# Kernel tuning notes

Measured on AMD Instinct MI355X. Metric: run time of the kernel, lower is better.

Reference implementation:

```python
import jax, jax.numpy as jnp
import numpy as np

B, S, D, H = 2, 2048, 1024, 16
HD = D // H  # head_dim = 64


def setup_inputs() -> dict:
    key = jax.random.key(0)
    ks = jax.random.split(key, 12)
    xav = (2.0 / (D + D)) ** 0.5  # xavier_normal std for square Linear
    q = jax.random.normal(ks[0], (B, S, D), jnp.float32)
    k = jax.random.normal(ks[1], (B, S, D), jnp.float32)
    v = jax.random.normal(ks[2], (B, S, D), jnp.float32)
    Wq = jax.random.normal(ks[3], (D, D), jnp.float32) * xav
    Wk = jax.random.normal(ks[4], (D, D), jnp.float32) * xav
    Wv = jax.random.normal(ks[5], (D, D), jnp.float32) * xav
    bq = jnp.zeros((D,), jnp.float32)
    bk = jnp.zeros((D,), jnp.float32)
    bv = jnp.zeros((D,), jnp.float32)
    # valid-prefix padding masks (True = valid token); key 0 always valid so
    # no causal softmax row is fully masked (avoids NaN, matches real usage).
    klen = jax.random.randint(ks[6], (B,), S // 2, S + 1)
    qlen = jax.random.randint(ks[7], (B,), S // 2, S + 1)
    pos = jnp.arange(S)
    key_padding_mask = pos[None, :] < klen[:, None]
    query_padding_mask = pos[None, :] < qlen[:, None]
    return {
        "q": q, "k": k, "v": v,
        "Wq": Wq, "bq": bq, "Wk": Wk, "bk": bk, "Wv": Wv, "bv": bv,
        "key_padding_mask": key_padding_mask,
        "query_padding_mask": query_padding_mask,
    }


def _proj_split(x, W, b, n_heads):
    # Linear (y = x W^T + b) then split heads: [B,S,D] -> [B,H,S,hd]
    bsz, sq, dm = x.shape
    hd = dm // n_heads
    y = x @ W.T + b
    return y.reshape(bsz, sq, n_heads, hd).transpose(0, 2, 1, 3)


def reference(q, k, v, Wq, bq, Wk, bk, Wv, bv, key_padding_mask, query_padding_mask):
    bsz, sq, dm = q.shape
    sk = k.shape[1]
    Q = _proj_split(q, Wq, bq, H)  # [B,H,Sq,hd]
    K = _proj_split(k, Wk, bk, H)  # [B,H,Sk,hd]
    V = _proj_split(v, Wv, bv, H)  # [B,H,Sk,hd]
    scale = 1.0 / jnp.sqrt(jnp.asarray(Q.shape[-1], Q.dtype))
    scores = jnp.einsum('bhqd,bhkd->bhqk', Q, K) * scale  # [B,H,Sq,Sk]
    # key padding: -inf where key invalid
    scores = jnp.where(key_padding_mask[:, None, None, :], scores, -jnp.inf)
    # causal: -inf strictly above the diagonal
    causal_ok = jnp.tril(jnp.ones((sq, sk), bool))
    scores = jnp.where(causal_ok[None, None, :, :], scores, -jnp.inf)
    attn = jax.nn.softmax(scores, axis=-1)
    # q_mask: zero out rows for padded queries (post-softmax, as in source)
    attn = jnp.where(query_padding_mask[:, None, :, None], attn, 0.0)
    # dropout p=0.0 -> identity
    out = jnp.einsum('bhqk,bhkd->bhqd', attn, V)
    out = out.transpose(0, 2, 1, 3).reshape(bsz, sq, dm)
    return out + q
```

## Files before the change

kernel.cpp:

```cpp
#include <hip/hip_runtime.h>
#include <stdint.h>

#define BATCH 2
#define SEQ 2048
#define DMODEL 1024
#define NHEAD 16
#define HDIM 64
#define CVT_BLOCKS 15360

typedef __attribute__((ext_vector_type(8))) short bf16x8;
typedef __attribute__((ext_vector_type(4))) float f32x4;

__device__ __forceinline__ unsigned short f2bf(float f) {
  unsigned int u = __float_as_uint(f);
  u += 0x7fffu + ((u >> 16) & 1u);
  return (unsigned short)(u >> 16);
}
__device__ __forceinline__ unsigned int pk2bf(float a, float b) {
  return __builtin_amdgcn_perm(__float_as_uint(b) + 0x8000u,
                               __float_as_uint(a) + 0x8000u, 0x07060302u);
}
__device__ __forceinline__ void async_copy16(const void* g, void* l) {
  __builtin_amdgcn_global_load_lds(
      (const __attribute__((address_space(1))) void*)g,
      (__attribute__((address_space(3))) void*)l, 16, 0, 0);
}

__global__ __launch_bounds__(256) void cvt_all(
    const float* __restrict__ q, const float* __restrict__ k,
    const float* __restrict__ v, const float* __restrict__ Wq,
    const float* __restrict__ Wk, const float* __restrict__ Wv,
    unsigned short* __restrict__ dst,
    const unsigned char* __restrict__ kp, const unsigned char* __restrict__ qp,
    int* __restrict__ lens) {
  if (blockIdx.x == CVT_BLOCKS) {
    const int t = threadIdx.x, wave = t >> 6, lane = t & 63;
    const unsigned char* base = (wave < 2) ? kp : qp;
    const int b = wave & 1;
    const bool bytefmt = (base[1] != 0);
    int cnt = 0;
    if (bytefmt) {
      const uint4* p = (const uint4*)(base + (size_t)b * SEQ);
#pragma unroll
      for (int g = 0; g < 2; g++) {
        const uint4 x = p[g * 64 + lane];
        const unsigned int w[4] = {x.x, x.y, x.z, x.w};
#pragma unroll
        for (int i = 0; i < 4; i++) {
          const unsigned int ww = w[i];
          cnt += ((ww & 0xffu) != 0) + ((ww & 0xff00u) != 0) +
                 ((ww & 0xff0000u) != 0) + ((ww & 0xff000000u) != 0);
        }
      }
    } else {
      const uint4* p = (const uint4*)(base + (size_t)b * SEQ * 4);
#pragma unroll
      for (int g = 0; g < 8; g++) {
        const uint4 x = p[g * 64 + lane];
        cnt += (x.x != 0) + (x.y != 0) + (x.z != 0) + (x.w != 0);
      }
    }
#pragma unroll
    for (int off = 32; off >= 1; off >>= 1) cnt += __shfl_xor(cnt, off, 64);
    if (lane == 0) lens[wave] = cnt;
    return;
  }
  const int g = blockIdx.x * 256 + threadIdx.x;
  const float* src;
  size_t off, dbase;
  if (g < 3 * (1 << 20)) {
    const int ti = g >> 20;
    src = (ti == 0) ? q : (ti == 1) ? k : v;
    off = (size_t)(g & ((1 << 20) - 1));
    dbase = (size_t)ti << 22;
  } else {
    const int gw = g - 3 * (1 << 20);
    const int ti = gw >> 18;
    src = (ti == 0) ? Wq : (ti == 1) ? Wk : Wv;
    off = (size_t)(gw & ((1 << 18) - 1));
    dbase = (3ull << 22) + ((size_t)ti << 20);
  }
  const float4 x = ((const float4*)src)[off];
  ushort4 o;
  o.x = f2bf(x.x); o.y = f2bf(x.y); o.z = f2bf(x.z); o.w = f2bf(x.w);
  *(ushort4*)(dst + dbase + off * 4) = o;
}

__global__ __launch_bounds__(256) void qkv_proj(
    const unsigned short* __restrict__ xq, const unsigned short* __restrict__ xk,
    const unsigned short* __restrict__ xv,
    const unsigned short* __restrict__ Wq, const float* __restrict__ bq,
    const unsigned short* __restrict__ Wk, const float* __restrict__ bk,
    const unsigned short* __restrict__ Wv, const float* __restrict__ bv,
    unsigned short* __restrict__ Qo, unsigned short* __restrict__ Ko,
    unsigned short* __restrict__ Vo, const int* __restrict__ lens) {
  const int z = blockIdx.z;
  const int m0 = blockIdx.y * 128, n0 = blockIdx.x * 128;
  const int b = m0 >> 11;
  const int len = (z == 0) ? lens[2 + b] : lens[b];
  if ((m0 & (SEQ - 1)) >= len) return;

  const unsigned short* x = (z == 0) ? xq : (z == 1) ? xk : xv;
  const unsigned short* W = (z == 0) ? Wq : (z == 1) ? Wk : Wv;
  const float* bias = (z == 0) ? bq : (z == 1) ? bk : bv;
  unsigned short* dst = (z == 0) ? Qo : (z == 1) ? Ko : Vo;
  const float osc = (z == 0) ? 0.18033688011112042f : 1.0f;

  __shared__ unsigned short As[128 * 64];
  __shared__ unsigned short Bs[128 * 64];

  const int t = threadIdx.x;
  const int wave = t >> 6, lane = t & 63, quad = lane >> 4, l16 = lane & 15;
  const int wm = wave >> 1, wn = wave & 1;

  const f32x4 fz = {0.f, 0.f, 0.f, 0.f};
  f32x4 acc[4][4];
#pragma unroll
  for (int i = 0; i < 4; i++)
#pragma unroll
    for (int j = 0; j < 4; j++) acc[i][j] = fz;

  for (int k0 = 0; k0 < DMODEL; k0 += 64) {
    __syncthreads();
#pragma unroll
    for (int c = 0; c < 4; c++) {
      const int slot = c * 256 + t;
      const int row = slot >> 3, pg = slot & 7;
      const int lg = (pg ^ (row & 7)) * 8;
      async_copy16(x + (size_t)(m0 + row) * DMODEL + k0 + lg,
                   (char*)As + (c * 256 + (t & 192)) * 16);
      async_copy16(W + (size_t)(n0 + row) * DMODEL + k0 + lg,
                   (char*)Bs + (c * 256 + (t & 192)) * 16);
    }
    __syncthreads();
#pragma unroll
    for (int kk = 0; kk < 2; kk++) {
      bf16x8 af[4], bfr[4];
#pragma unroll
      for (int i = 0; i < 4; i++) {
        const int ra = wm * 64 + i * 16 + l16;
        const int rb = wn * 64 + i * 16 + l16;
        af[i] = *(const bf16x8*)(As + ra * 64 + ((kk * 4 + quad) ^ (ra & 7)) * 8);
        bfr[i] = *(const bf16x8*)(Bs + rb * 64 + ((kk * 4 + quad) ^ (rb & 7)) * 8);
      }
      if (z == 2) {
#pragma unroll
        for (int i = 0; i < 4; i++)
#pragma unroll
          for (int j = 0; j < 4; j++)
            acc[i][j] = __builtin_amdgcn_mfma_f32_16x16x32_bf16(af[i], bfr[j], acc[i][j], 0, 0, 0);
      } else {
#pragma unroll
        for (int i = 0; i < 4; i++)
#pragma unroll
          for (int j = 0; j < 4; j++)
            acc[i][j] = __builtin_amdgcn_mfma_f32_16x16x32_bf16(bfr[j], af[i], acc[i][j], 0, 0, 0);
      }
    }
  }

  if (z == 2) {
#pragma unroll
    for (int j = 0; j < 4; j++) {
      const int n = n0 + wn * 64 + j * 16 + l16;
      const float bb_ = bias[n];
      const int h = n >> 6, hd = n & 63;
#pragma unroll
      for (int i = 0; i < 4; i++) {
        const int s0 = (m0 & (SEQ - 1)) + wm * 64 + i * 16 + quad * 4;
        uint2 w;
        w.x = pk2bf(acc[i][j][0] + bb_, acc[i][j][1] + bb_);
        w.y = pk2bf(acc[i][j][2] + bb_, acc[i][j][3] + bb_);
        *(uint2*)(dst + (((size_t)(b * NHEAD + h) * HDIM + hd) << 11) + s0) = w;
      }
    }
  } else {
#pragma unroll
    for (int j = 0; j < 4; j++) {
      const int nb = n0 + wn * 64 + j * 16 + quad * 4;
      const float4 b4 = *(const float4*)(bias + nb);
      const int h = nb >> 6, hd0 = nb & 63;
#pragma unroll
      for (int i = 0; i < 4; i++) {
        const int s = (m0 & (SEQ - 1)) + wm * 64 + i * 16 + l16;
        uint2 w;
        w.x = pk2bf((acc[i][j][0] + b4.x) * osc, (acc[i][j][1] + b4.y) * osc);
        w.y = pk2bf((acc[i][j][2] + b4.z) * osc, (acc[i][j][3] + b4.w) * osc);
        *(uint2*)(dst + (((size_t)(b * NHEAD + h) * SEQ + s) << 6) + hd0) = w;
      }
    }
  }
}


#define KVB 64

template <bool MASKED>
__device__ __forceinline__ void softmax_update(
    const f32x4 s[4], int key0, int qrow, int klen, int quad, int l16,
    float& mst, float& lsum, f32x4 o[4], unsigned short* Pdst) {
  float pm[4][4];
  float rm = -__builtin_inff();
  if (MASKED) {
    const int kmax = ((qrow < klen - 1) ? qrow : klen - 1) - key0 - quad * 4;
#pragma unroll
    for (int nf = 0; nf < 4; nf++)
#pragma unroll
      for (int r = 0; r < 4; r++) {
        pm[nf][r] = (nf * 16 + r <= kmax) ? s[nf][r] : -__builtin_inff();
        rm = fmaxf(rm, pm[nf][r]);
      }
  } else {
#pragma unroll
    for (int nf = 0; nf < 4; nf++)
#pragma unroll
      for (int r = 0; r < 4; r++) {
        pm[nf][r] = s[nf][r];
        rm = fmaxf(rm, pm[nf][r]);
      }
  }
  rm = fmaxf(rm, __shfl_xor(rm, 16, 64));
  rm = fmaxf(rm, __shfl_xor(rm, 32, 64));
  if (__ballot(rm > mst + 8.0f) != 0ull) {
    const float mnew = fmaxf(mst, rm);
    const float alpha = exp2f(fmaxf(mst, -1e30f) - fmaxf(mnew, -1e30f));
    mst = mnew;
    lsum *= alpha;
    float ab[4];
#pragma unroll
    for (int r = 0; r < 4; r++) ab[r] = __shfl(alpha, quad * 4 + r, 64);
#pragma unroll
    for (int db = 0; db < 4; db++)
#pragma unroll
      for (int r = 0; r < 4; r++) o[db][r] *= ab[r];
  }
  const float mref = fmaxf(mst, -1e30f);
  float rs = 0.f;
#pragma unroll
  for (int nf = 0; nf < 4; nf++)
#pragma unroll
    for (int r = 0; r < 4; r++) {
      const float p = exp2f(pm[nf][r] - mref);
      pm[nf][r] = p;
      rs += p;
    }
  rs += __shfl_xor(rs, 16, 64);
  rs += __shfl_xor(rs, 32, 64);
  lsum += rs;
#pragma unroll
  for (int nf = 0; nf < 4; nf++) {
    uint2 w;
    w.x = pk2bf(pm[nf][0], pm[nf][1]);
    w.y = pk2bf(pm[nf][2], pm[nf][3]);
    const int g = (nf * 2 + (quad >> 1)) ^ (l16 & 7);
    *(uint2*)(Pdst + l16 * KVB + g * 8 + (quad & 1) * 4) = w;
  }
}

template <bool MASKED>
__device__ __forceinline__ void tile_pass(
    const unsigned short* __restrict__ ks, const unsigned short* __restrict__ vt,
    unsigned short* __restrict__ Pw, bf16x8 qf0, bf16x8 qf1,
    int key0, int qrow, int klen, int quad, int l16,
    float& mst, float& lsum, f32x4 o[4]) {
  const f32x4 fz = {0.f, 0.f, 0.f, 0.f};
  f32x4 s[4];
  __builtin_amdgcn_s_setprio(1);
#pragma unroll
  for (int nf = 0; nf < 4; nf++) {
    const int row = nf * 16 + l16;
    const int sw = row & 7;
    const bf16x8 kf0 = *(const bf16x8*)(ks + row * 64 + (quad ^ sw) * 8);
    const bf16x8 kf1 = *(const bf16x8*)(ks + row * 64 + ((quad + 4) ^ sw) * 8);
    f32x4 a = fz;
    a = __builtin_amdgcn_mfma_f32_16x16x32_bf16(kf0, qf0, a, 0, 0, 0);
    a = __builtin_amdgcn_mfma_f32_16x16x32_bf16(kf1, qf1, a, 0, 0, 0);
    s[nf] = a;
  }
  __builtin_amdgcn_s_setprio(0);
  softmax_update<MASKED>(s, key0, qrow, klen, quad, l16, mst, lsum, o, Pw);
  bf16x8 pf[2];
#pragma unroll
  for (int ksn = 0; ksn < 2; ksn++)
    pf[ksn] = *(const bf16x8*)(Pw + l16 * KVB + ((ksn * 4 + quad) ^ (l16 & 7)) * 8);
  __builtin_amdgcn_s_setprio(1);
#pragma unroll
  for (int db = 0; db < 4; db++) {
    const int d = db * 16 + l16;
    const int sw = d & 7;
#pragma unroll
    for (int ksn = 0; ksn < 2; ksn++) {
      const bf16x8 v = *(const bf16x8*)(vt + d * KVB + ((ksn * 4 + quad) ^ sw) * 8);
      o[db] = __builtin_amdgcn_mfma_f32_16x16x32_bf16(pf[ksn], v, o[db], 0, 0, 0);
    }
  }
  __builtin_amdgcn_s_setprio(0);
}

__global__ __launch_bounds__(256, 4) void attn_kernel(
    const unsigned short* __restrict__ Qb, const unsigned short* __restrict__ Kb,
    const unsigned short* __restrict__ VTb, const float* __restrict__ qin,
    const int* __restrict__ lens, float* __restrict__ out) {
  const int tile = blockIdx.x, h = blockIdx.y, b = blockIdx.z;
  const int bh = b * NHEAD + h;
  const int t = threadIdx.x, wave = t >> 6, lane = t & 63, quad = lane >> 4, l16 = lane & 15;
  const int klen = lens[b], qlen = lens[2 + b];

  __shared__ unsigned short Ks[2][KVB * 64];
  __shared__ unsigned short VT[2][KVB * 64];
  __shared__ unsigned short Ps[4][16 * KVB];

  const unsigned short* Qp = Qb + (size_t)bh * SEQ * HDIM;
  const unsigned short* Kp = Kb + (size_t)bh * SEQ * HDIM;
  const unsigned short* Vt = VTb + (size_t)bh * HDIM * SEQ;

  const int qrow = tile * 64 + wave * 16 + l16;
  const bf16x8 qf0 = *(const bf16x8*)(Qp + (size_t)qrow * HDIM + quad * 8);
  const bf16x8 qf1 = *(const bf16x8*)(Qp + (size_t)qrow * HDIM + 32 + quad * 8);

  const f32x4 fz = {0.f, 0.f, 0.f, 0.f};
  f32x4 o[4];
#pragma unroll
  for (int i = 0; i < 4; i++) o[i] = fz;
  float mst = -__builtin_inff(), lsum = 0.f;

  int ktot = 0;
  if (tile * 64 < qlen) {
    const int kend = ((tile * 64 + 64) < klen) ? (tile * 64 + 64) : klen;
    ktot = (kend + 63) >> 6;
  }

  auto STAGE = [&](int buf, int kt) {
    const int key0 = kt << 6;
#pragma unroll
    for (int u = 0; u < 2; u++) {
      const int c = u * 256 + t;
      const int row = c >> 3;
      const int sg = ((t & 7) ^ (row & 7)) * 8;
      async_copy16(Kp + (size_t)(key0 + row) * HDIM + sg,
                   (char*)Ks[buf] + (u * 256 + (t & 192)) * 16);
      async_copy16(Vt + (size_t)row * SEQ + key0 + sg,
                   (char*)VT[buf] + (u * 256 + (t & 192)) * 16);
    }
  };

  if (ktot > 0) {
    STAGE(0, 0);
    __syncthreads();
    int cur = 0;
    for (int kt = 0; kt < ktot; kt++) {
      if (kt + 1 < ktot) STAGE(cur ^ 1, kt + 1);
      const int key0 = kt << 6;
      if ((key0 + 63 <= tile * 64 + wave * 16) && (key0 + 63 < klen))
        tile_pass<false>(Ks[cur], VT[cur], Ps[wave], qf0, qf1, key0, qrow,
                         klen, quad, l16, mst, lsum, o);
      else
        tile_pass<true>(Ks[cur], VT[cur], Ps[wave], qf0, qf1, key0, qrow,
                        klen, quad, l16, mst, lsum, o);
      __syncthreads();
      cur ^= 1;
    }
  }

  const float inv = (lsum > 0.f) ? 1.f / lsum : 0.f;
  float ib[4];
#pragma unroll
  for (int r = 0; r < 4; r++) ib[r] = __shfl(inv, quad * 4 + r, 64);
#pragma unroll
  for (int db = 0; db < 4; db++) {
    const int col = h * HDIM + db * 16 + l16;
#pragma unroll
    for (int r = 0; r < 4; r++) {
      const int i = tile * 64 + wave * 16 + quad * 4 + r;
      const size_t oo = (size_t)(b * SEQ + i) * DMODEL + col;
      out[oo] = ((i < qlen) ? o[db][r] * ib[r] : 0.f) + qin[oo];
    }
  }
}

extern "C" void kernel_launch(void* const* d_in, const int* in_sizes, int n_in,
                              void* d_out, int out_size, void* d_ws, size_t ws_size,
                              hipStream_t stream) {
  (void)in_sizes; (void)n_in; (void)out_size; (void)ws_size;
  const float* q = (const float*)d_in[0];
  const float* k = (const float*)d_in[1];
  const float* v = (const float*)d_in[2];
  const float* Wq = (const float*)d_in[3];
  const float* bq = (const float*)d_in[4];
  const float* Wk = (const float*)d_in[5];
  const float* bk = (const float*)d_in[6];
  const float* Wv = (const float*)d_in[7];
  const float* bv = (const float*)d_in[8];
  const unsigned char* kpm = (const unsigned char*)d_in[9];
  const unsigned char* qpm = (const unsigned char*)d_in[10];
  float* out = (float*)d_out;

  const size_t tsz = (size_t)BATCH * SEQ * DMODEL;
  const size_t wsz = (size_t)DMODEL * DMODEL;

  char* ws = (char*)d_ws;
  int* lens = (int*)ws;
  unsigned short* cvt_base = (unsigned short*)(ws + 256);
  unsigned short* qb16 = cvt_base;
  unsigned short* kb16 = qb16 + tsz;
  unsigned short* vb16 = kb16 + tsz;
  unsigned short* Wqb = vb16 + tsz;
  unsigned short* Wkb = Wqb + wsz;
  unsigned short* Wvb = Wkb + wsz;
  unsigned short* Qw = Wvb + wsz;
  unsigned short* Kw = Qw + tsz;
  unsigned short* Vtw = Kw + tsz;

  cvt_all<<<dim3(CVT_BLOCKS + 1), dim3(256), 0, stream>>>(q, k, v, Wq, Wk, Wv,
                                                          cvt_base, kpm, qpm, lens);
  qkv_proj<<<dim3(8, 32, 3), dim3(256), 0, stream>>>(qb16, kb16, vb16, Wqb, bq, Wkb, bk, Wvb, bv, Qw, Kw, Vtw, lens);
  attn_kernel<<<dim3(32, NHEAD, BATCH), dim3(256), 0, stream>>>(Qw, Kw, Vtw, q, lens, out);
}
```

Before: 217.4 us.

## Split attention KV loop across two wave groups with split-K merge

After: 221.1 us. No clear change (+1.7%).

```diff
diff --git a/kernel.cpp b/kernel.cpp
--- a/kernel.cpp
+++ b/kernel.cpp
@@ -194,6 +194,7 @@
 
 
 #define KVB 64
+#define KPAIR 128
 
 template <bool MASKED>
 __device__ __forceinline__ void softmax_update(
@@ -260,7 +261,7 @@
 template <bool MASKED>
 __device__ __forceinline__ void tile_pass(
     const unsigned short* __restrict__ ks, const unsigned short* __restrict__ vt,
-    unsigned short* __restrict__ Pw, bf16x8 qf0, bf16x8 qf1,
+    int vgbase, unsigned short* __restrict__ Pw, bf16x8 qf0, bf16x8 qf1,
     int key0, int qrow, int klen, int quad, int l16,
     float& mst, float& lsum, f32x4 o[4]) {
   const f32x4 fz = {0.f, 0.f, 0.f, 0.f};
@@ -287,34 +288,35 @@
 #pragma unroll
   for (int db = 0; db < 4; db++) {
     const int d = db * 16 + l16;
-    const int sw = d & 7;
 #pragma unroll
     for (int ksn = 0; ksn < 2; ksn++) {
-      const bf16x8 v = *(const bf16x8*)(vt + d * KVB + ((ksn * 4 + quad) ^ sw) * 8);
+      const bf16x8 v =
+          *(const bf16x8*)(vt + d * KPAIR + ((vgbase + ksn * 4 + quad) ^ l16) * 8);
       o[db] = __builtin_amdgcn_mfma_f32_16x16x32_bf16(pf[ksn], v, o[db], 0, 0, 0);
     }
   }
   __builtin_amdgcn_s_setprio(0);
 }
 
-__global__ __launch_bounds__(256, 4) void attn_kernel(
+__global__ __launch_bounds__(512, 4) void attn_kernel(
     const unsigned short* __restrict__ Qb, const unsigned short* __restrict__ Kb,
     const unsigned short* __restrict__ VTb, const float* __restrict__ qin,
     const int* __restrict__ lens, float* __restrict__ out) {
   const int tile = blockIdx.x, h = blockIdx.y, b = blockIdx.z;
   const int bh = b * NHEAD + h;
   const int t = threadIdx.x, wave = t >> 6, lane = t & 63, quad = lane >> 4, l16 = lane & 15;
+  const int grp = wave >> 2, w4 = wave & 3;
   const int klen = lens[b], qlen = lens[2 + b];
 
-  __shared__ unsigned short Ks[2][KVB * 64];
-  __shared__ unsigned short VT[2][KVB * 64];
-  __shared__ unsigned short Ps[4][16 * KVB];
+  __shared__ unsigned short Ks[2][KPAIR * 64];
+  __shared__ unsigned short VT[2][64 * KPAIR];
+  __shared__ unsigned short Ps[8][16 * KVB];
 
   const unsigned short* Qp = Qb + (size_t)bh * SEQ * HDIM;
   const unsigned short* Kp = Kb + (size_t)bh * SEQ * HDIM;
   const unsigned short* Vt = VTb + (size_t)bh * HDIM * SEQ;
 
-  const int qrow = tile * 64 + wave * 16 + l16;
+  const int qrow = tile * 64 + w4 * 16 + l16;
   const bf16x8 qf0 = *(const bf16x8*)(Qp + (size_t)qrow * HDIM + quad * 8);
   const bf16x8 qf1 = *(const bf16x8*)(Qp + (size_t)qrow * HDIM + 32 + quad * 8);
 
@@ -324,56 +326,94 @@
   for (int i = 0; i < 4; i++) o[i] = fz;
   float mst = -__builtin_inff(), lsum = 0.f;
 
-  int ktot = 0;
+  int nk = 0;
   if (tile * 64 < qlen) {
     const int kend = ((tile * 64 + 64) < klen) ? (tile * 64 + 64) : klen;
-    ktot = (kend + 63) >> 6;
-  }
-
-  auto STAGE = [&](int buf, int kt) {
-    const int key0 = kt << 6;
-#pragma unroll
-    for (int u = 0; u < 2; u++) {
-      const int c = u * 256 + t;
-      const int row = c >> 3;
-      const int sg = ((t & 7) ^ (row & 7)) * 8;
-      async_copy16(Kp + (size_t)(key0 + row) * HDIM + sg,
-                   (char*)Ks[buf] + (u * 256 + (t & 192)) * 16);
-      async_copy16(Vt + (size_t)row * SEQ + key0 + sg,
-                   (char*)VT[buf] + (u * 256 + (t & 192)) * 16);
+    nk = (kend + 63) >> 6;
+  }
+  const int npair = (nk + 1) >> 1;
+
+  auto STAGE = [&](int buf, int j) {
+    const int key0 = j << 7;
+#pragma unroll
+    for (int c = 0; c < 2; c++) {
+      const int slot = c * 512 + t;
+      const int krow = slot >> 3;
+      const int kg = ((slot & 7) ^ (krow & 7)) * 8;
+      async_copy16(Kp + (size_t)(key0 + krow) * HDIM + kg,
+                   (char*)Ks[buf] + (c * 512 + (t & 448)) * 16);
+      const int vrow = slot >> 4;
+      const int vg = ((slot & 15) ^ (vrow & 15)) * 8;
+      async_copy16(Vt + (size_t)vrow * SEQ + key0 + vg,
+                   (char*)VT[buf] + (c * 512 + (t & 448)) * 16);
     }
   };
 
-  if (ktot > 0) {
-    STAGE(0, 0);
-    __syncthreads();
-    int cur = 0;
-    for (int kt = 0; kt < ktot; kt++) {
-      if (kt + 1 < ktot) STAGE(cur ^ 1, kt + 1);
-      const int key0 = kt << 6;
-      if ((key0 + 63 <= tile * 64 + wave * 16) && (key0 + 63 < klen))
-        tile_pass<false>(Ks[cur], VT[cur], Ps[wave], qf0, qf1, key0, qrow,
+  if (npair > 0) STAGE(0, 0);
+  __syncthreads();
+  int cur = 0;
+  const unsigned short* ksg_off[1];
+  (void)ksg_off;
+  for (int j = 0; j < npair; j++) {
+    if (j + 1 < npair) STAGE(cur ^ 1, j + 1);
+    const int myIdx = 2 * j + grp;
+    if (myIdx < nk) {
+      const int key0 = myIdx << 6;
+      const unsigned short* ksg = Ks[cur] + grp * 64 * 64;
+      if ((key0 + 63 <= tile * 64 + w4 * 16) && (key0 + 63 < klen))
+        tile_pass<false>(ksg, VT[cur], grp * 8, Ps[wave], qf0, qf1, key0, qrow,
                          klen, quad, l16, mst, lsum, o);
       else
-        tile_pass<true>(Ks[cur], VT[cur], Ps[wave], qf0, qf1, key0, qrow,
+        tile_pass<true>(ksg, VT[cur], grp * 8, Ps[wave], qf0, qf1, key0, qrow,
                         klen, quad, l16, mst, lsum, o);
-      __syncthreads();
-      cur ^= 1;
-    }
-  }
-
-  const float inv = (lsum > 0.f) ? 1.f / lsum : 0.f;
-  float ib[4];
-#pragma unroll
-  for (int r = 0; r < 4; r++) ib[r] = __shfl(inv, quad * 4 + r, 64);
-#pragma unroll
-  for (int db = 0; db < 4; db++) {
-    const int col = h * HDIM + db * 16 + l16;
+    }
+    __syncthreads();
+    cur ^= 1;
+  }
+
+  float* sc = (float*)Ks;
+  if (grp == 1) {
+    float* w = sc + ((size_t)(w4 * 64 + lane)) * 18;
+    w[0] = mst;
+    w[1] = lsum;
+#pragma unroll
+    for (int db = 0; db < 4; db++)
+#pragma unroll
+      for (int r = 0; r < 4; r++) w[2 + db * 4 + r] = o[db][r];
+  }
+  __syncthreads();
+  if (grp == 0) {
+    const float* w = sc + ((size_t)(w4 * 64 + lane)) * 18;
+    const float m1 = w[0], l1 = w[1];
+    const float mN = fmaxf(mst, m1);
+    const float a0 = exp2f(fmaxf(mst, -1e30f) - fmaxf(mN, -1e30f));
+    const float a1 = exp2f(fmaxf(m1, -1e30f) - fmaxf(mN, -1e30f));
+    lsum = lsum * a0 + l1 * a1;
+    float ab0[4], ab1[4];
 #pragma unroll
     for (int r = 0; r < 4; r++) {
-      const int i = tile * 64 + wave * 16 + quad * 4 + r;
-      const size_t oo = (size_t)(b * SEQ + i) * DMODEL + col;
-      out[oo] = ((i < qlen) ? o[db][r] * ib[r] : 0.f) + qin[oo];
+      ab0[r] = __shfl(a0, quad * 4 + r, 64);
+      ab1[r] = __shfl(a1, quad * 4 + r, 64);
+    }
+#pragma unroll
+    for (int db = 0; db < 4; db++)
+#pragma unroll
+      for (int r = 0; r < 4; r++)
+        o[db][r] = o[db][r] * ab0[r] + w[2 + db * 4 + r] * ab1[r];
+
+    const float inv = (lsum > 0.f) ? 1.f / lsum : 0.f;
+    float ib[4];
+#pragma unroll
+    for (int r = 0; r < 4; r++) ib[r] = __shfl(inv, quad * 4 + r, 64);
+#pragma unroll
+    for (int db = 0; db < 4; db++) {
+      const int col = h * HDIM + db * 16 + l16;
+#pragma unroll
+      for (int r = 0; r < 4; r++) {
+        const int i = tile * 64 + w4 * 16 + quad * 4 + r;
+        const size_t oo = (size_t)(b * SEQ + i) * DMODEL + col;
+        out[oo] = ((i < qlen) ? o[db][r] * ib[r] : 0.f) + qin[oo];
+      }
     }
   }
 }
@@ -414,5 +454,5 @@
   cvt_all<<<dim3(CVT_BLOCKS + 1), dim3(256), 0, stream>>>(q, k, v, Wq, Wk, Wv,
                                                           cvt_base, kpm, qpm, lens);
   qkv_proj<<<dim3(8, 32, 3), dim3(256), 0, stream>>>(qb16, kb16, vb16, Wqb, bq, Wkb, bk, Wvb, bv, Qw, Kw, Vtw, lens);
-  attn_kernel<<<dim3(32, NHEAD, BATCH), dim3(256), 0, stream>>>(Qw, Kw, Vtw, q, lens, out);
-}
+  attn_kernel<<<dim3(32, NHEAD, BATCH), dim3(512), 0, stream>>>(Qw, Kw, Vtw, q, lens, out);
+}
```

## Switch attention to 32x32 MFMA tiles with register-resident P and 128-row query blocks

Applied to the files above, without the earlier changes.

New measurement: 415.5 us. +91.1%, slower.

```diff
diff --git a/kernel.cpp b/kernel.cpp
--- a/kernel.cpp
+++ b/kernel.cpp
@@ -10,6 +10,8 @@
 
 typedef __attribute__((ext_vector_type(8))) short bf16x8;
 typedef __attribute__((ext_vector_type(4))) float f32x4;
+typedef __attribute__((ext_vector_type(16))) float f32x16;
+typedef __attribute__((ext_vector_type(4))) unsigned int u32x4;
 
 __device__ __forceinline__ unsigned short f2bf(float f) {
   unsigned int u = __float_as_uint(f);
@@ -19,6 +21,11 @@
 __device__ __forceinline__ unsigned int pk2bf(float a, float b) {
   return __builtin_amdgcn_perm(__float_as_uint(b) + 0x8000u,
                                __float_as_uint(a) + 0x8000u, 0x07060302u);
+}
+__device__ __forceinline__ unsigned int cvtpk(float lo, float hi) {
+  unsigned int r;
+  asm("v_cvt_pk_bf16_f32 %0, %1, %2" : "=v"(r) : "v"(lo), "v"(hi));
+  return r;
 }
 __device__ __forceinline__ void async_copy16(const void* g, void* l) {
   __builtin_amdgcn_global_load_lds(
@@ -196,102 +203,97 @@
 #define KVB 64
 
 template <bool MASKED>
-__device__ __forceinline__ void softmax_update(
-    const f32x4 s[4], int key0, int qrow, int klen, int quad, int l16,
-    float& mst, float& lsum, f32x4 o[4], unsigned short* Pdst) {
-  float pm[4][4];
+__device__ __forceinline__ void tile_pass32(
+    const unsigned short* __restrict__ ks, const unsigned short* __restrict__ vt,
+    const bf16x8 (&qf)[4], int key0, int q0, int l31, int hi, int klen,
+    float& mst, float& lsum, f32x16 (&o)[2]) {
+  const f32x16 fz16 = {0.f, 0.f, 0.f, 0.f, 0.f, 0.f, 0.f, 0.f,
+                       0.f, 0.f, 0.f, 0.f, 0.f, 0.f, 0.f, 0.f};
+  f32x16 s[2] = {fz16, fz16};
+  __builtin_amdgcn_s_setprio(1);
+#pragma unroll
+  for (int tt = 0; tt < 2; tt++) {
+    const int row = tt * 32 + l31;
+    const int sw = row & 7;
+#pragma unroll
+    for (int dk = 0; dk < 4; dk++) {
+      const bf16x8 kf = *(const bf16x8*)(ks + row * 64 + (((dk * 2 + hi) ^ sw) * 8));
+      s[tt] = __builtin_amdgcn_mfma_f32_32x32x16_bf16(kf, qf[dk], s[tt], 0, 0, 0);
+    }
+  }
+  __builtin_amdgcn_s_setprio(0);
+
   float rm = -__builtin_inff();
   if (MASKED) {
-    const int kmax = ((qrow < klen - 1) ? qrow : klen - 1) - key0 - quad * 4;
-#pragma unroll
-    for (int nf = 0; nf < 4; nf++)
-#pragma unroll
-      for (int r = 0; r < 4; r++) {
-        pm[nf][r] = (nf * 16 + r <= kmax) ? s[nf][r] : -__builtin_inff();
-        rm = fmaxf(rm, pm[nf][r]);
+    const int qq = q0 + l31;
+    const int kmaxl = ((qq < klen - 1) ? qq : (klen - 1)) - key0 - 4 * hi;
+#pragma unroll
+    for (int tt = 0; tt < 2; tt++)
+#pragma unroll
+      for (int r = 0; r < 16; r++) {
+        const int kk = tt * 32 + (r & 3) + 8 * (r >> 2);
+        if (kk > kmaxl) s[tt][r] = -__builtin_inff();
+        rm = fmaxf(rm, s[tt][r]);
       }
   } else {
 #pragma unroll
-    for (int nf = 0; nf < 4; nf++)
-#pragma unroll
-      for (int r = 0; r < 4; r++) {
-        pm[nf][r] = s[nf][r];
-        rm = fmaxf(rm, pm[nf][r]);
-      }
-  }
-  rm = fmaxf(rm, __shfl_xor(rm, 16, 64));
+    for (int tt = 0; tt < 2; tt++)
+#pragma unroll
+      for (int r = 0; r < 16; r++) rm = fmaxf(rm, s[tt][r]);
+  }
   rm = fmaxf(rm, __shfl_xor(rm, 32, 64));
   if (__ballot(rm > mst + 8.0f) != 0ull) {
-    const float mnew = fmaxf(mst, rm);
-    const float alpha = exp2f(fmaxf(mst, -1e30f) - fmaxf(mnew, -1e30f));
-    mst = mnew;
-    lsum *= alpha;
-    float ab[4];
-#pragma unroll
-    for (int r = 0; r < 4; r++) ab[r] = __shfl(alpha, quad * 4 + r, 64);
-#pragma unroll
-    for (int db = 0; db < 4; db++)
-#pragma unroll
-      for (int r = 0; r < 4; r++) o[db][r] *= ab[r];
+    const float mn = fmaxf(mst, rm);
+    const float al = exp2f(fmaxf(mst, -1e30f) - fmaxf(mn, -1e30f));
+    mst = mn;
+    lsum *= al;
+#pragma unroll
+    for (int r = 0; r < 16; r++) {
+      const float ar = __shfl(al, (r & 3) + 8 * (r >> 2) + 4 * hi, 64);
+      o[0][r] *= ar;
+      o[1][r] *= ar;
+    }
   }
   const float mref = fmaxf(mst, -1e30f);
   float rs = 0.f;
 #pragma unroll
-  for (int nf = 0; nf < 4; nf++)
-#pragma unroll
-    for (int r = 0; r < 4; r++) {
-      const float p = exp2f(pm[nf][r] - mref);
-      pm[nf][r] = p;
+  for (int tt = 0; tt < 2; tt++)
+#pragma unroll
+    for (int r = 0; r < 16; r++) {
+      const float p = exp2f(s[tt][r] - mref);
+      s[tt][r] = p;
       rs += p;
     }
-  rs += __shfl_xor(rs, 16, 64);
   rs += __shfl_xor(rs, 32, 64);
   lsum += rs;
-#pragma unroll
-  for (int nf = 0; nf < 4; nf++) {
-    uint2 w;
-    w.x = pk2bf(pm[nf][0], pm[nf][1]);
-    w.y = pk2bf(pm[nf][2], pm[nf][3]);
-    const int g = (nf * 2 + (quad >> 1)) ^ (l16 & 7);
-    *(uint2*)(Pdst + l16 * KVB + g * 8 + (quad & 1) * 4) = w;
-  }
-}
-
-template <bool MASKED>
-__device__ __forceinline__ void tile_pass(
-    const unsigned short* __restrict__ ks, const unsigned short* __restrict__ vt,
-    unsigned short* __restrict__ Pw, bf16x8 qf0, bf16x8 qf1,
-    int key0, int qrow, int klen, int quad, int l16,
-    float& mst, float& lsum, f32x4 o[4]) {
-  const f32x4 fz = {0.f, 0.f, 0.f, 0.f};
-  f32x4 s[4];
+
+  unsigned int Ac[8], Bc[8];
+#pragma unroll
+  for (int c = 0; c < 8; c++) {
+    const int tt = c >> 2, rb = (c & 3) << 2;
+    Ac[c] = cvtpk(s[tt][rb + 0], s[tt][rb + 1]);
+    Bc[c] = cvtpk(s[tt][rb + 2], s[tt][rb + 3]);
+  }
   __builtin_amdgcn_s_setprio(1);
 #pragma unroll
-  for (int nf = 0; nf < 4; nf++) {
-    const int row = nf * 16 + l16;
-    const int sw = row & 7;
-    const bf16x8 kf0 = *(const bf16x8*)(ks + row * 64 + (quad ^ sw) * 8);
-    const bf16x8 kf1 = *(const bf16x8*)(ks + row * 64 + ((quad + 4) ^ sw) * 8);
-    f32x4 a = fz;
-    a = __builtin_amdgcn_mfma_f32_16x16x32_bf16(kf0, qf0, a, 0, 0, 0);
-    a = __builtin_amdgcn_mfma_f32_16x16x32_bf16(kf1, qf1, a, 0, 0, 0);
-    s[nf] = a;
-  }
-  __builtin_amdgcn_s_setprio(0);
-  softmax_update<MASKED>(s, key0, qrow, klen, quad, l16, mst, lsum, o, Pw);
-  bf16x8 pf[2];
-#pragma unroll
-  for (int ksn = 0; ksn < 2; ksn++)
-    pf[ksn] = *(const bf16x8*)(Pw + l16 * KVB + ((ksn * 4 + quad) ^ (l16 & 7)) * 8);
-  __builtin_amdgcn_s_setprio(1);
-#pragma unroll
-  for (int db = 0; db < 4; db++) {
-    const int d = db * 16 + l16;
-    const int sw = d & 7;
-#pragma unroll
-    for (int ksn = 0; ksn < 2; ksn++) {
-      const bf16x8 v = *(const bf16x8*)(vt + d * KVB + ((ksn * 4 + quad) ^ sw) * 8);
-      o[db] = __builtin_amdgcn_mfma_f32_16x16x32_bf16(pf[ksn], v, o[db], 0, 0, 0);
+  for (int ksn = 0; ksn < 4; ksn++) {
+    const unsigned int pA0 = (unsigned int)__shfl_xor((int)Ac[2 * ksn], 32, 64);
+    const unsigned int pB0 = (unsigned int)__shfl_xor((int)Bc[2 * ksn], 32, 64);
+    const unsigned int pA1 = (unsigned int)__shfl_xor((int)Ac[2 * ksn + 1], 32, 64);
+    const unsigned int pB1 = (unsigned int)__shfl_xor((int)Bc[2 * ksn + 1], 32, 64);
+    u32x4 w;
+    w[0] = hi ? pA1 : Ac[2 * ksn];
+    w[1] = hi ? pB1 : Bc[2 * ksn];
+    w[2] = hi ? Ac[2 * ksn + 1] : pA0;
+    w[3] = hi ? Bc[2 * ksn + 1] : pB0;
+    bf16x8 pa;
+    __builtin_memcpy(&pa, &w, 16);
+#pragma unroll
+    for (int dt = 0; dt < 2; dt++) {
+      const int d = dt * 32 + l31;
+      const bf16x8 v =
+          *(const bf16x8*)(vt + d * 64 + (((ksn * 2 + hi) ^ (d & 7)) * 8));
+      o[dt] = __builtin_amdgcn_mfma_f32_32x32x16_bf16(pa, v, o[dt], 0, 0, 0);
     }
   }
   __builtin_amdgcn_s_setprio(0);
@@ -301,79 +303,84 @@
     const unsigned short* __restrict__ Qb, const unsigned short* __restrict__ Kb,
     const unsigned short* __restrict__ VTb, const float* __restrict__ qin,
     const int* __restrict__ lens, float* __restrict__ out) {
-  const int tile = blockIdx.x, h = blockIdx.y, b = blockIdx.z;
+  const int tile = 15 - blockIdx.x;
+  const int h = blockIdx.y, b = blockIdx.z;
   const int bh = b * NHEAD + h;
-  const int t = threadIdx.x, wave = t >> 6, lane = t & 63, quad = lane >> 4, l16 = lane & 15;
+  const int t = threadIdx.x, wv = t >> 6, lane = t & 63;
+  const int l31 = lane & 31, hi = lane >> 5;
   const int klen = lens[b], qlen = lens[2 + b];
+  const int q0 = tile * 128 + wv * 32;
 
   __shared__ unsigned short Ks[2][KVB * 64];
   __shared__ unsigned short VT[2][KVB * 64];
-  __shared__ unsigned short Ps[4][16 * KVB];
 
   const unsigned short* Qp = Qb + (size_t)bh * SEQ * HDIM;
   const unsigned short* Kp = Kb + (size_t)bh * SEQ * HDIM;
   const unsigned short* Vt = VTb + (size_t)bh * HDIM * SEQ;
 
-  const int qrow = tile * 64 + wave * 16 + l16;
-  const bf16x8 qf0 = *(const bf16x8*)(Qp + (size_t)qrow * HDIM + quad * 8);
-  const bf16x8 qf1 = *(const bf16x8*)(Qp + (size_t)qrow * HDIM + 32 + quad * 8);
-
-  const f32x4 fz = {0.f, 0.f, 0.f, 0.f};
-  f32x4 o[4];
-#pragma unroll
-  for (int i = 0; i < 4; i++) o[i] = fz;
+  bf16x8 qf[4];
+#pragma unroll
+  for (int dk = 0; dk < 4; dk++)
+    qf[dk] = *(const bf16x8*)(Qp + (size_t)(q0 + l31) * HDIM + dk * 16 + hi * 8);
+
+  const f32x16 fz16 = {0.f, 0.f, 0.f, 0.f, 0.f, 0.f, 0.f, 0.f,
+                       0.f, 0.f, 0.f, 0.f, 0.f, 0.f, 0.f, 0.f};
+  f32x16 o[2] = {fz16, fz16};
   float mst = -__builtin_inff(), lsum = 0.f;
 
-  int ktot = 0;
-  if (tile * 64 < qlen) {
-    const int kend = ((tile * 64 + 64) < klen) ? (tile * 64 + 64) : klen;
-    ktot = (kend + 63) >> 6;
+  int ktot = 0, myi = 0;
+  if (tile * 128 < qlen) {
+    const int ke = ((tile * 128 + 128) < klen) ? (tile * 128 + 128) : klen;
+    ktot = (ke + 63) >> 6;
+  }
+  if (q0 < qlen) {
+    const int ke = ((q0 + 32) < klen) ? (q0 + 32) : klen;
+    myi = (ke + 63) >> 6;
   }
 
   auto STAGE = [&](int buf, int kt) {
     const int key0 = kt << 6;
 #pragma unroll
-    for (int u = 0; u < 2; u++) {
-      const int c = u * 256 + t;
-      const int row = c >> 3;
-      const int sg = ((t & 7) ^ (row & 7)) * 8;
+    for (int c = 0; c < 2; c++) {
+      const int slot = c * 256 + t;
+      const int row = slot >> 3, ch = slot & 7;
+      const int sg = (ch ^ (row & 7)) * 8;
       async_copy16(Kp + (size_t)(key0 + row) * HDIM + sg,
-                   (char*)Ks[buf] + (u * 256 + (t & 192)) * 16);
+                   (char*)Ks[buf] + (c * 256 + (t & 192)) * 16);
       async_copy16(Vt + (size_t)row * SEQ + key0 + sg,
-                   (char*)VT[buf] + (u * 256 + (t & 192)) * 16);
+                   (char*)VT[buf] + (c * 256 + (t & 192)) * 16);
     }
   };
 
-  if (ktot > 0) {
-    STAGE(0, 0);
+  if (ktot > 0) STAGE(0, 0);
+  __syncthreads();
+  int cur = 0;
+  for (int kt = 0; kt < ktot; kt++) {
+    if (kt + 1 < ktot) STAGE(cur ^ 1, kt + 1);
+    if (kt < myi) {
+      const int key0 = kt << 6;
+      if ((key0 + 63 <= q0) && (key0 + 64 <= klen))
+        tile_pass32<false>(Ks[cur], VT[cur], qf, key0, q0, l31, hi, klen,
+                           mst, lsum, o);
+      else
+        tile_pass32<true>(Ks[cur], VT[cur], qf, key0, q0, l31, hi, klen,
+                          mst, lsum, o);
+    }
     __syncthreads();
-    int cur = 0;
-    for (int kt = 0; kt < ktot; kt++) {
-      if (kt + 1 < ktot) STAGE(cur ^ 1, kt + 1);
-      const int key0 = kt << 6;
-      if ((key0 + 63 <= tile * 64 + wave * 16) && (key0 + 63 < klen))
-        tile_pass<false>(Ks[cur], VT[cur], Ps[wave], qf0, qf1, key0, qrow,
-                         klen, quad, l16, mst, lsum, o);
-      else
-        tile_pass<true>(Ks[cur], VT[cur], Ps[wave], qf0, qf1, key0, qrow,
-                        klen, quad, l16, mst, lsum, o);
-      __syncthreads();
-      cur ^= 1;
-    }
+    cur ^= 1;
   }
 
   const float inv = (lsum > 0.f) ? 1.f / lsum : 0.f;
-  float ib[4];
-#pragma unroll
-  for (int r = 0; r < 4; r++) ib[r] = __shfl(inv, quad * 4 + r, 64);
-#pragma unroll
-  for (int db = 0; db < 4; db++) {
-    const int col = h * HDIM + db * 16 + l16;
-#pragma unroll
-    for (int r = 0; r < 4; r++) {
-      const int i = tile * 64 + wave * 16 + quad * 4 + r;
-      const size_t oo = (size_t)(b * SEQ + i) * DMODEL + col;
-      out[oo] = ((i < qlen) ? o[db][r] * ib[r] : 0.f) + qin[oo];
+#pragma unroll
+  for (int r = 0; r < 16; r++) {
+    const int cr = (r & 3) + 8 * (r >> 2) + 4 * hi;
+    const float iv = __shfl(inv, cr, 64);
+    const int qq = q0 + cr;
+#pragma unroll
+    for (int dt = 0; dt < 2; dt++) {
+      const int col = h * HDIM + dt * 32 + l31;
+      const size_t oo = (size_t)(b * SEQ + qq) * DMODEL + col;
+      out[oo] = ((qq < qlen) ? o[dt][r] * iv : 0.f) + qin[oo];
     }
   }
 }
@@ -414,5 +421,5 @@
   cvt_all<<<dim3(CVT_BLOCKS + 1), dim3(256), 0, stream>>>(q, k, v, Wq, Wk, Wv,
                                                           cvt_base, kpm, qpm, lens);
   qkv_proj<<<dim3(8, 32, 3), dim3(256), 0, stream>>>(qb16, kb16, vb16, Wqb, bq, Wkb, bk, Wvb, bv, Qw, Kw, Vtw, lens);
-  attn_kernel<<<dim3(32, NHEAD, BATCH), dim3(256), 0, stream>>>(Qw, Kw, Vtw, q, lens, out);
-}
+  attn_kernel<<<dim3(16, NHEAD, BATCH), dim3(256), 0, stream>>>(Qw, Kw, Vtw, q, lens, out);
+}
```
